# Kernel optimization log

Measured on AMD Instinct MI355X. Metric: run time of the kernel, lower is better.

The kernel has to match this reference:

```python
import jax, jax.numpy as jnp
import numpy as np

N_HEAD = 16


def setup_inputs() -> dict:
    key = jax.random.key(0)
    k1, k2, k3 = jax.random.split(key, 3)
    B, S, D = 2, 2048, 1024
    return {
        "hidden_states": jax.random.normal(k1, (B, S, D), dtype=jnp.float32),
        "c_attn_w": jax.random.normal(k2, (D, 3 * D), dtype=jnp.float32) * 0.02,
        "c_attn_b": jnp.zeros((3 * D,), dtype=jnp.float32),
        "c_proj_w": jax.random.normal(k3, (D, D), dtype=jnp.float32) * 0.02,
        "c_proj_b": jnp.zeros((D,), dtype=jnp.float32),
    }


def reference(hidden_states, c_attn_w, c_attn_b, c_proj_w, c_proj_b):
    B, S, D = hidden_states.shape
    H = N_HEAD
    hd = D // H
    # Fused QKV projection (Conv1D == linear with transposed weight layout)
    qkv = hidden_states @ c_attn_w + c_attn_b  # [B,S,3D]
    q, k, v = jnp.split(qkv, 3, axis=-1)
    # split heads -> [B,H,S,hd]
    q = q.reshape(B, S, H, hd).transpose(0, 2, 1, 3)
    k = k.reshape(B, S, H, hd).transpose(0, 2, 1, 3)
    v = v.reshape(B, S, H, hd).transpose(0, 2, 1, 3)
    # scaled dot-product with causal mask
    scores = jnp.einsum("bhqd,bhkd->bhqk", q, k) / jnp.asarray(hd ** 0.5, q.dtype)
    causal = jnp.tril(jnp.ones((S, S), dtype=bool))  # [S,S]
    mask_value = jnp.finfo(scores.dtype).min
    scores = jnp.where(causal[None, None, :, :], scores, mask_value)
    attn_weights = jax.nn.softmax(scores, axis=-1)  # [B,H,S,S]
    ctx = jnp.einsum("bhqk,bhkd->bhqd", attn_weights, v)  # [B,H,S,hd]
    ctx = ctx.transpose(0, 2, 1, 3).reshape(B, S, D)  # merge heads
    out = ctx @ c_proj_w + c_proj_b  # [B,S,D]
    return out
```

## Files before the change

### kernel.cpp

```cpp
#include <hip/hip_runtime.h>
#include <hip/hip_bf16.h>

typedef __attribute__((ext_vector_type(8))) short short8;
typedef __attribute__((ext_vector_type(4))) float f32x4;
typedef __attribute__((ext_vector_type(16))) float f32x16;
typedef __attribute__((ext_vector_type(4))) unsigned short u16x4;
typedef __attribute__((ext_vector_type(4))) unsigned int u32x4;

#define MFMA16(a, b, c) __builtin_amdgcn_mfma_f32_16x16x32_bf16((a), (b), (c), 0, 0, 0)
#define MFMA32(a, b, c) __builtin_amdgcn_mfma_f32_32x32x16_bf16((a), (b), (c), 0, 0, 0)

__device__ __forceinline__ unsigned short f2bf(float f) {
    union { float f; unsigned u; } v; v.f = f;
    return (unsigned short)((v.u + 0x7fffu + ((v.u >> 16) & 1u)) >> 16);
}

__device__ __forceinline__ unsigned cvtpk(float lo, float hi_) {
    unsigned r;
    asm volatile("v_cvt_pk_bf16_f32 %0, %1, %2" : "=v"(r) : "v"(lo), "v"(hi_));
    return r;
}

__global__ void cast_x_kernel(const float* __restrict__ x, ushort* __restrict__ y) {
    int i = blockIdx.x * blockDim.x + threadIdx.x;
    float4 v = ((const float4*)x)[i];
    u16x4 o = { f2bf(v.x), f2bf(v.y), f2bf(v.z), f2bf(v.w) };
    *(u16x4*)(y + (size_t)i * 4) = o;
}

__global__ void transpose_cast_kernel(const float* __restrict__ W, ushort* __restrict__ WT,
                                      int K, int N) {
    __shared__ ushort t[64][66];
    int n0 = blockIdx.x * 64, k0 = blockIdx.y * 64;
    int tn = threadIdx.x & 63, tg = threadIdx.x >> 6;
#pragma unroll
    for (int i = 0; i < 16; ++i) {
        int k = tg * 16 + i;
        t[tn][k] = f2bf(W[(size_t)(k0 + k) * N + n0 + tn]);
    }
    __syncthreads();
#pragma unroll
    for (int i = 0; i < 16; ++i) {
        int nn = tg * 16 + i;
        WT[(size_t)(n0 + nn) * K + k0 + tn] = t[nn][tn];
    }
}

#define QSCALE 0.18033688011112042f

template <int MODE>
__global__ __launch_bounds__(256, 3)
void gemm_bt_kernel(const ushort* __restrict__ A, const ushort* __restrict__ BT,
                    const float* __restrict__ bias,
                    ushort* __restrict__ Qb, ushort* __restrict__ Kb,
                    ushort* __restrict__ VT, float* __restrict__ Out,
                    int M, int N, int K) {
    __shared__ ushort Asm[2][128 * 32];
    __shared__ ushort Bsm[2][128 * 32];
    const int tid = threadIdx.x;
    const int lane = tid & 63;
    const int wv = tid >> 6;
    const int l15 = lane & 15, lg = lane >> 4;
    const int rm = (wv >> 1) * 64, cn = (wv & 1) * 64;
    const int row0 = blockIdx.y * 128, col0 = blockIdx.x * 128;

    const char* Agb = (const char*)(A + (size_t)row0 * K);
    const char* Bgb = (const char*)(BT + (size_t)col0 * K);
    const size_t rowbytes = (size_t)K * 2;

    f32x4 acc[4][4];
#pragma unroll
    for (int mi = 0; mi < 4; ++mi)
#pragma unroll
        for (int ni = 0; ni < 4; ++ni) acc[mi][ni] = f32x4{0.f, 0.f, 0.f, 0.f};

    const int sr0 = tid >> 2, sc0 = (tid & 3) ^ (sr0 & 3);
    const int sr1 = (tid + 256) >> 2, sc1 = (tid & 3) ^ (sr1 & 3);

#define GSTAGE(buf, k0_)                                                                \
    do {                                                                                \
        size_t kbyte = (size_t)(k0_)*2;                                                 \
        __builtin_amdgcn_global_load_lds(                                               \
            (const __attribute__((address_space(1))) void*)(Agb + (size_t)sr0 *         \
                rowbytes + kbyte + sc0 * 16),                                           \
            (__attribute__((address_space(3))) void*)((char*)&Asm[buf][0] + tid * 16),  \
            16, 0, 0);                                                                  \
        __builtin_amdgcn_global_load_lds(                                               \
            (const __attribute__((address_space(1))) void*)(Agb + (size_t)sr1 *         \
                rowbytes + kbyte + sc1 * 16),                                           \
            (__attribute__((address_space(3))) void*)((char*)&Asm[buf][0] + 4096 +      \
                tid * 16),                                                              \
            16, 0, 0);                                                                  \
        __builtin_amdgcn_global_load_lds(                                               \
            (const __attribute__((address_space(1))) void*)(Bgb + (size_t)sr0 *         \
                rowbytes + kbyte + sc0 * 16),                                           \
            (__attribute__((address_space(3))) void*)((char*)&Bsm[buf][0] + tid * 16),  \
            16, 0, 0);                                                                  \
        __builtin_amdgcn_global_load_lds(                                               \
            (const __attribute__((address_space(1))) void*)(Bgb + (size_t)sr1 *         \
                rowbytes + kbyte + sc1 * 16),                                           \
            (__attribute__((address_space(3))) void*)((char*)&Bsm[buf][0] + 4096 +      \
                tid * 16),                                                              \
            16, 0, 0);                                                                  \
    } while (0)

    GSTAGE(0, 0);
    __syncthreads();

    const int sw8 = (lg ^ (l15 & 3)) << 3;

    int cur = 0;
    for (int k0 = 0; k0 < K; k0 += 32) {
        if (k0 + 32 < K) GSTAGE(cur ^ 1, k0 + 32);
        short8 af[4], bf[4];
#pragma unroll
        for (int mi = 0; mi < 4; ++mi)
            af[mi] = *(const short8*)&Asm[cur][(rm + mi * 16 + l15) * 32 + sw8];
#pragma unroll
        for (int ni = 0; ni < 4; ++ni)
            bf[ni] = *(const short8*)&Bsm[cur][(cn + ni * 16 + l15) * 32 + sw8];
        __builtin_amdgcn_s_setprio(1);
#pragma unroll
        for (int mi = 0; mi < 4; ++mi)
#pragma unroll
            for (int ni = 0; ni < 4; ++ni)
                acc[mi][ni] = MFMA16(af[mi], bf[ni], acc[mi][ni]);
        __builtin_amdgcn_s_setprio(0);
        __syncthreads();
        cur ^= 1;
    }
#undef GSTAGE

    if (MODE == 0) {
        const int sect = col0 >> 10;
#pragma unroll
        for (int ni = 0; ni < 4; ++ni) {
            int col = col0 + cn + ni * 16 + l15;
            float bv = bias[col];
            int dcol = col & 1023, h = dcol >> 6, dd = dcol & 63;
#pragma unroll
            for (int mi = 0; mi < 4; ++mi) {
                int mrow0 = row0 + rm + mi * 16 + lg * 4;
                if (sect == 2) {
                    int b = mrow0 >> 11, s = mrow0 & 2047;
                    u16x4 o;
#pragma unroll
                    for (int j = 0; j < 4; ++j) o[j] = f2bf(acc[mi][ni][j] + bv);
                    *(u16x4*)&VT[((size_t)((b << 4) + h) * 64 + dd) * 2048 + s] = o;
                } else {
                    ushort* dst = sect ? Kb : Qb;
                    float sc = sect ? 1.f : QSCALE;
#pragma unroll
                    for (int j = 0; j < 4; ++j) {
                        int tok = mrow0 + j;
                        int b = tok >> 11, s = tok & 2047;
                        dst[((size_t)((b << 4) + h) * 2048 + s) * 64 + dd] =
                            f2bf((acc[mi][ni][j] + bv) * sc);
                    }
                }
            }
        }
    } else {
#pragma unroll
        for (int ni = 0; ni < 4; ++ni) {
            int col = col0 + cn + ni * 16 + l15;
            float bv = bias[col];
#pragma unroll
            for (int mi = 0; mi < 4; ++mi) {
                int mrow0 = row0 + rm + mi * 16 + lg * 4;
#pragma unroll
                for (int j = 0; j < 4; ++j)
                    Out[(size_t)(mrow0 + j) * N + col] = acc[mi][ni][j] + bv;
            }
        }
    }
}

template <int SPLIT>
__global__ __launch_bounds__(256, 4)
void attn_kernel(const ushort* __restrict__ Qb, const ushort* __restrict__ Kb,
                 const ushort* __restrict__ VT, ushort* __restrict__ CTX,
                 float* __restrict__ OP, float* __restrict__ ML) {
    __shared__ __align__(16) ushort Ksm[2][64 * 64];
    __shared__ __align__(16) ushort Vsm[2][64 * 64];

    const int tid = threadIdx.x;
    const int lane = tid & 63;
    const int w = tid >> 6;
    const int l31 = lane & 31;
    const int hi = lane >> 5;
    const int r7 = l31 & 7;

    const int id = blockIdx.x;
    int bh, qt, half, cBeg, cEnd;
    if (SPLIT) {
        const int xcd = id & 7, jj = id >> 3;
        bh = (xcd << 2) + (jj & 3);
        const int r = jj >> 2;
        half = r >> 4;
        const int s = r & 15;
        qt = (s < 8) ? s : 23 - s;
        cBeg = half * (qt + 1);
        cEnd = cBeg + (qt + 1);
    } else {
        const int xcd = id & 7, jj = id >> 3;
        bh = (xcd << 2) + (jj >> 4);
        qt = ((jj >> 5) & 1) ? (jj & 15) : 15 - (jj & 15);
        half = 0; cBeg = 0; cEnd = 2 * qt + 2;
    }
    const int nc = 2 * qt + 2;
    const int qw0 = qt * 128 + w * 32;
    const int qrow = qw0 + l31;

    const ushort* Qh = Qb + (size_t)bh * 2048 * 64;
    const ushort* Kh = Kb + (size_t)bh * 2048 * 64;
    const ushort* Vh = VT + (size_t)bh * 64 * 2048;

    short8 qf[4];
#pragma unroll
    for (int dc = 0; dc < 4; ++dc)
        qf[dc] = *(const short8*)&Qh[(size_t)qrow * 64 + dc * 16 + hi * 8];

    const int srow = tid >> 3;
    const int sxor = ((tid & 7) ^ (srow & 7)) * 8;

#define GLL(src, dst) __builtin_amdgcn_global_load_lds(                                 \
        (const __attribute__((address_space(1))) void*)(src),                           \
        (__attribute__((address_space(3))) void*)(dst), 16, 0, 0)

#define STAGE(buf, kb_)                                                                 \
    do {                                                                                \
        const ushort* kp = Kh + (size_t)((kb_) + srow) * 64 + sxor;                     \
        GLL(kp, (char*)&Ksm[buf][0] + tid * 16);                                        \
        GLL(kp + 32 * 64, (char*)&Ksm[buf][0] + 4096 + tid * 16);                       \
        const ushort* vp = Vh + (size_t)srow * 2048 + (kb_) + sxor;                     \
        GLL(vp, (char*)&Vsm[buf][0] + tid * 16);                                        \
        GLL(vp + (size_t)32 * 2048, (char*)&Vsm[buf][0] + 4096 + tid * 16);             \
    } while (0)

    const int cdiag = 2 * qt + (w >> 1);

    STAGE(0, cBeg * 64);
    __syncthreads();

    float mrun = -1e30f, lsum = 0.f;
    f32x16 acc0, acc1;
#pragma unroll
    for (int r = 0; r < 16; ++r) { acc0[r] = 0.f; acc1[r] = 0.f; }

    int cur = 0;
    for (int c = cBeg; c < cEnd; ++c) {
        const int kb = c * 64;
        if (c + 1 < cEnd) STAGE(cur ^ 1, kb + 64);

        if (!(w < 2 && c == nc - 1)) {
            const ushort* Kc = &Ksm[cur][0];
            const ushort* Vc = &Vsm[cur][0];

            f32x16 st0, st1;
#pragma unroll
            for (int r = 0; r < 16; ++r) { st0[r] = 0.f; st1[r] = 0.f; }
            __builtin_amdgcn_s_setprio(1);
#pragma unroll
            for (int dc = 0; dc < 4; ++dc) {
                short8 kf0 = *(const short8*)(Kc + l31 * 64 + (((dc * 2 + hi) ^ r7) << 3));
                short8 kf1 = *(const short8*)(Kc + (32 + l31) * 64 + (((dc * 2 + hi) ^ r7) << 3));
                st0 = MFMA32(kf0, qf[dc], st0);
                st1 = MFMA32(kf1, qf[dc], st1);
            }
            __builtin_amdgcn_s_setprio(0);

            if (c == cdiag) {
                const int base0 = kb + (hi << 2);
                const int base1 = kb + 32 + (hi << 2);
#pragma unroll
                for (int r = 0; r < 16; ++r) {
                    int k0 = base0 + ((r & 3) + 8 * (r >> 2));
                    int k1 = base1 + ((r & 3) + 8 * (r >> 2));
                    st0[r] = (k0 <= qrow) ? st0[r] : -1e30f;
                    st1[r] = (k1 <= qrow) ? st1[r] : -1e30f;
                }
            }

            float tm[8];
#pragma unroll
            for (int i = 0; i < 8; ++i)
                tm[i] = fmaxf(fmaxf(st0[i], st0[i + 8]), fmaxf(st1[i], st1[i + 8]));
            float tmax = fmaxf(fmaxf(fmaxf(tm[0], tm[1]), fmaxf(tm[2], tm[3])),
                               fmaxf(fmaxf(tm[4], tm[5]), fmaxf(tm[6], tm[7])));
            tmax = fmaxf(tmax, __shfl_xor(tmax, 32));

            if (!__all(tmax <= mrun + 8.0f)) {
                float mnew = fmaxf(mrun, tmax);
                float sc = exp2f(mrun - mnew);
#pragma unroll
                for (int r = 0; r < 16; ++r) { acc0[r] *= sc; acc1[r] *= sc; }
                lsum *= sc;
                mrun = mnew;
            }

#pragma unroll
            for (int r = 0; r < 16; ++r) st0[r] = exp2f(st0[r] - mrun);
#pragma unroll
            for (int r = 0; r < 16; ++r) st1[r] = exp2f(st1[r] - mrun);
            float ts[8];
#pragma unroll
            for (int i = 0; i < 8; ++i) ts[i] = st0[i] + st0[i + 8];
#pragma unroll
            for (int i = 0; i < 8; ++i) ts[i] += st1[i] + st1[i + 8];
            float tsum = ((ts[0] + ts[1]) + (ts[2] + ts[3])) +
                         ((ts[4] + ts[5]) + (ts[6] + ts[7]));
            lsum += tsum;

#define MAKE_PFRAG(st, kcL, out)                                                        \
    do {                                                                                \
        unsigned a0 = cvtpk(st[8 * kcL + 0], st[8 * kcL + 1]);                          \
        unsigned a1 = cvtpk(st[8 * kcL + 2], st[8 * kcL + 3]);                          \
        unsigned b0 = cvtpk(st[8 * kcL + 4], st[8 * kcL + 5]);                          \
        unsigned b1 = cvtpk(st[8 * kcL + 6], st[8 * kcL + 7]);                          \
        asm volatile("v_permlane32_swap_b32 %0, %1" : "+v"(a0), "+v"(b0));              \
        asm volatile("v_permlane32_swap_b32 %0, %1" : "+v"(a1), "+v"(b1));              \
        u32x4 fw;                                                                       \
        fw.x = a0; fw.y = a1; fw.z = b0; fw.w = b1;                                     \
        out = __builtin_bit_cast(short8, fw);                                           \
    } while (0)

#define PV_GROUP(st, kcL, g)                                                            \
    do {                                                                                \
        short8 pf;                                                                      \
        MAKE_PFRAG(st, kcL, pf);                                                        \
        short8 v0 = *(const short8*)(Vc + l31 * 64 + (((2 * (g) + hi) ^ r7) << 3));     \
        short8 v1 = *(const short8*)(Vc + (32 + l31) * 64 +                             \
                                     (((2 * (g) + hi) ^ r7) << 3));                     \
        acc0 = MFMA32(v0, pf, acc0);                                                    \
        acc1 = MFMA32(v1, pf, acc1);                                                    \
    } while (0)

            __builtin_amdgcn_s_setprio(1);
            PV_GROUP(st0, 0, 0);
            PV_GROUP(st0, 1, 1);
            PV_GROUP(st1, 0, 2);
            PV_GROUP(st1, 1, 3);
            __builtin_amdgcn_s_setprio(0);
#undef PV_GROUP
#undef MAKE_PFRAG
        }

        __syncthreads();
        cur ^= 1;
    }
#undef STAGE
#undef GLL

    lsum += __shfl_xor(lsum, 32);

    if (SPLIT) {
        const int pidx = ((bh << 4) + qt) * 2 + half;
        float* op = OP + (size_t)pidx * 8192 + (size_t)(w * 32 + l31) * 64;
#define WRITE_PART(accv, dt)                                                            \
    do {                                                                                \
        _Pragma("unroll")                                                               \
        for (int q2 = 0; q2 < 4; ++q2) {                                                \
            int d0 = dt * 32 + 8 * q2 + (hi << 2);                                      \
            f32x4 o = { accv[4 * q2 + 0], accv[4 * q2 + 1],                             \
                        accv[4 * q2 + 2], accv[4 * q2 + 3] };                           \
            *(f32x4*)&op[d0] = o;                                                       \
        }                                                                               \
    } while (0)
        WRITE_PART(acc0, 0);
        WRITE_PART(acc1, 1);
#undef WRITE_PART
        if (hi == 0) {
            float2 r2 = { mrun, lsum };
            *(float2*)&ML[((size_t)pidx * 128 + w * 32 + l31) * 2] = r2;
        }
    } else {
        const float inv = 1.f / lsum;
        const int b = bh >> 4, h = bh & 15;
        const size_t tokrow = ((size_t)b * 2048 + qw0 + l31) * 1024 + (size_t)h * 64;
#define WRITE_DT(accv, dt)                                                              \
    do {                                                                                \
        _Pragma("unroll")                                                               \
        for (int q2 = 0; q2 < 4; ++q2) {                                                \
            int d0 = dt * 32 + 8 * q2 + (hi << 2);                                      \
            u16x4 o;                                                                    \
            _Pragma("unroll")                                                           \
            for (int j = 0; j < 4; ++j) o[j] = f2bf(accv[4 * q2 + j] * inv);            \
            *(u16x4*)&CTX[tokrow + d0] = o;                                             \
        }                                                                               \
    } while (0)
        WRITE_DT(acc0, 0);
        WRITE_DT(acc1, 1);
#undef WRITE_DT
    }
}

__global__ __launch_bounds__(256)
void merge_kernel(const float* __restrict__ OP, const float* __restrict__ ML,
                  ushort* __restrict__ CTX) {
    const int bid = blockIdx.x;
    const int bh = bid >> 4, qt = bid & 15;
    const int tid = threadIdx.x;
    const int row = tid >> 1, dh = (tid & 1) << 5;
    const size_t p0 = (size_t)bid * 2, p1 = p0 + 1;
    const float2 ml0 = *(const float2*)&ML[(p0 * 128 + row) * 2];
    const float2 ml1 = *(const float2*)&ML[(p1 * 128 + row) * 2];
    const float M = fmaxf(ml0.x, ml1.x);
    const float f0 = exp2f(ml0.x - M), f1 = exp2f(ml1.x - M);
    const float inv = 1.f / (f0 * ml0.y + f1 * ml1.y);
    const float* a0 = OP + p0 * 8192 + (size_t)row * 64 + dh;
    const float* a1 = OP + p1 * 8192 + (size_t)row * 64 + dh;
    const size_t tok = (size_t)(bh >> 4) * 2048 + qt * 128 + row;
    ushort* dst = CTX + tok * 1024 + (size_t)(bh & 15) * 64 + dh;
#pragma unroll
    for (int k = 0; k < 8; ++k) {
        f32x4 v0 = *(const f32x4*)(a0 + 4 * k);
        f32x4 v1 = *(const f32x4*)(a1 + 4 * k);
        u16x4 o;
#pragma unroll
        for (int j = 0; j < 4; ++j) o[j] = f2bf((f0 * v0[j] + f1 * v1[j]) * inv);
        *(u16x4*)(dst + 4 * k) = o;
    }
}

extern "C" void kernel_launch(void* const* d_in, const int* in_sizes, int n_in,
                              void* d_out, int out_size, void* d_ws, size_t ws_size,
                              hipStream_t stream) {
    const float* X     = (const float*)d_in[0];
    const float* Wqkv  = (const float*)d_in[1];
    const float* bqkv  = (const float*)d_in[2];
    const float* Wproj = (const float*)d_in[3];
    const float* bproj = (const float*)d_in[4];
    float* Out = (float*)d_out;

    ushort* Xb     = (ushort*)d_ws;
    ushort* WqkvT  = Xb + (size_t)4096 * 1024;
    ushort* WprojT = WqkvT + (size_t)3072 * 1024;
    ushort* Qb     = WprojT + (size_t)1024 * 1024;
    ushort* Kb     = Qb + (size_t)4096 * 1024;
    ushort* VT     = Kb + (size_t)4096 * 1024;
    ushort* CTX    = VT + (size_t)4096 * 1024;
    float* OP = (float*)((char*)d_ws + (size_t)48 * 1024 * 1024);
    float* ML = OP + (size_t)1024 * 128 * 64;
    const size_t NEED = (size_t)(48 + 32 + 1) * 1024 * 1024;

    cast_x_kernel<<<4096, 256, 0, stream>>>(X, Xb);
    transpose_cast_kernel<<<dim3(48, 16), 256, 0, stream>>>(Wqkv, WqkvT, 1024, 3072);
    transpose_cast_kernel<<<dim3(16, 16), 256, 0, stream>>>(Wproj, WprojT, 1024, 1024);
    gemm_bt_kernel<0><<<dim3(24, 32), 256, 0, stream>>>(Xb, WqkvT, bqkv, Qb, Kb, VT, nullptr,
                                                        4096, 3072, 1024);
    if (ws_size >= NEED) {
        attn_kernel<1><<<1024, 256, 0, stream>>>(Qb, Kb, VT, CTX, OP, ML);
        merge_kernel<<<512, 256, 0, stream>>>(OP, ML, CTX);
    } else {
        attn_kernel<0><<<512, 256, 0, stream>>>(Qb, Kb, VT, CTX, nullptr, nullptr);
    }
    gemm_bt_kernel<1><<<dim3(8, 32), 256, 0, stream>>>(CTX, WprojT, bproj, nullptr, nullptr,
                                                       nullptr, Out, 4096, 1024, 1024);
}
```

Measured before the change: 131.6 us.

## Triple-buffer GEMM loads, store split-attention partials in bf16, vectorize merge

The GEMM main loop moves from double to triple-buffered LDS staging. It uses explicit vmcnt waits and a single barrier per iteration, so global loads run two stages ahead of the MFMA work. The split-K attention partial outputs are now written as bf16 instead of fp32, which halves the traffic to and from the partial buffer. The merge kernel is rewritten to use 16-byte vector loads and stores. In exchange, partials lose precision before the merge, and the GEMM uses more LDS, which may reduce occupancy.

```diff
diff --git a/kernel.cpp b/kernel.cpp
--- a/kernel.cpp
+++ b/kernel.cpp
@@ -5,6 +5,7 @@
 typedef __attribute__((ext_vector_type(4))) float f32x4;
 typedef __attribute__((ext_vector_type(16))) float f32x16;
 typedef __attribute__((ext_vector_type(4))) unsigned short u16x4;
+typedef __attribute__((ext_vector_type(8))) unsigned short u16x8;
 typedef __attribute__((ext_vector_type(4))) unsigned int u32x4;
 
 #define MFMA16(a, b, c) __builtin_amdgcn_mfma_f32_16x16x32_bf16((a), (b), (c), 0, 0, 0)
@@ -13,6 +14,11 @@
 __device__ __forceinline__ unsigned short f2bf(float f) {
     union { float f; unsigned u; } v; v.f = f;
     return (unsigned short)((v.u + 0x7fffu + ((v.u >> 16) & 1u)) >> 16);
+}
+
+__device__ __forceinline__ float bf2f(unsigned short s) {
+    union { unsigned u; float f; } v; v.u = (unsigned)s << 16;
+    return v.f;
 }
 
 __device__ __forceinline__ unsigned cvtpk(float lo, float hi_) {
@@ -55,8 +61,8 @@
                     ushort* __restrict__ Qb, ushort* __restrict__ Kb,
                     ushort* __restrict__ VT, float* __restrict__ Out,
                     int M, int N, int K) {
-    __shared__ ushort Asm[2][128 * 32];
-    __shared__ ushort Bsm[2][128 * 32];
+    __shared__ ushort Asm[3][128 * 32];
+    __shared__ ushort Bsm[3][128 * 32];
     const int tid = threadIdx.x;
     const int lane = tid & 63;
     const int wv = tid >> 6;
@@ -104,14 +110,18 @@
             16, 0, 0);                                                                  \
     } while (0)
 
+    const int NK = K >> 5;
     GSTAGE(0, 0);
-    __syncthreads();
+    GSTAGE(1, 32);
 
     const int sw8 = (lg ^ (l15 & 3)) << 3;
 
-    int cur = 0;
-    for (int k0 = 0; k0 < K; k0 += 32) {
-        if (k0 + 32 < K) GSTAGE(cur ^ 1, k0 + 32);
+    int cur = 0, stg = 2;
+    for (int i = 0; i < NK; ++i) {
+        if (i < NK - 1) asm volatile("s_waitcnt vmcnt(4)" ::: "memory");
+        else            asm volatile("s_waitcnt vmcnt(0)" ::: "memory");
+        __builtin_amdgcn_s_barrier();
+        if (i + 2 < NK) GSTAGE(stg, (i + 2) * 32);
         short8 af[4], bf[4];
 #pragma unroll
         for (int mi = 0; mi < 4; ++mi)
@@ -126,8 +136,8 @@
             for (int ni = 0; ni < 4; ++ni)
                 acc[mi][ni] = MFMA16(af[mi], bf[ni], acc[mi][ni]);
         __builtin_amdgcn_s_setprio(0);
-        __syncthreads();
-        cur ^= 1;
+        cur = (cur == 2) ? 0 : cur + 1;
+        stg = (stg == 2) ? 0 : stg + 1;
     }
 #undef GSTAGE
 
@@ -180,7 +190,7 @@
 __global__ __launch_bounds__(256, 4)
 void attn_kernel(const ushort* __restrict__ Qb, const ushort* __restrict__ Kb,
                  const ushort* __restrict__ VT, ushort* __restrict__ CTX,
-                 float* __restrict__ OP, float* __restrict__ ML) {
+                 ushort* __restrict__ OP, float* __restrict__ ML) {
     __shared__ __align__(16) ushort Ksm[2][64 * 64];
     __shared__ __align__(16) ushort Vsm[2][64 * 64];
 
@@ -356,15 +366,16 @@
 
     if (SPLIT) {
         const int pidx = ((bh << 4) + qt) * 2 + half;
-        float* op = OP + (size_t)pidx * 8192 + (size_t)(w * 32 + l31) * 64;
+        ushort* op = OP + (size_t)pidx * 8192 + (size_t)(w * 32 + l31) * 64;
 #define WRITE_PART(accv, dt)                                                            \
     do {                                                                                \
         _Pragma("unroll")                                                               \
         for (int q2 = 0; q2 < 4; ++q2) {                                                \
             int d0 = dt * 32 + 8 * q2 + (hi << 2);                                      \
-            f32x4 o = { accv[4 * q2 + 0], accv[4 * q2 + 1],                             \
-                        accv[4 * q2 + 2], accv[4 * q2 + 3] };                           \
-            *(f32x4*)&op[d0] = o;                                                       \
+            u16x4 o;                                                                    \
+            _Pragma("unroll")                                                           \
+            for (int j = 0; j < 4; ++j) o[j] = f2bf(accv[4 * q2 + j]);                  \
+            *(u16x4*)&op[d0] = o;                                                       \
         }                                                                               \
     } while (0)
         WRITE_PART(acc0, 0);
@@ -396,30 +407,30 @@
 }
 
 __global__ __launch_bounds__(256)
-void merge_kernel(const float* __restrict__ OP, const float* __restrict__ ML,
+void merge_kernel(const ushort* __restrict__ OP, const float* __restrict__ ML,
                   ushort* __restrict__ CTX) {
     const int bid = blockIdx.x;
     const int bh = bid >> 4, qt = bid & 15;
     const int tid = threadIdx.x;
-    const int row = tid >> 1, dh = (tid & 1) << 5;
-    const size_t p0 = (size_t)bid * 2, p1 = p0 + 1;
-    const float2 ml0 = *(const float2*)&ML[(p0 * 128 + row) * 2];
-    const float2 ml1 = *(const float2*)&ML[(p1 * 128 + row) * 2];
-    const float M = fmaxf(ml0.x, ml1.x);
-    const float f0 = exp2f(ml0.x - M), f1 = exp2f(ml1.x - M);
-    const float inv = 1.f / (f0 * ml0.y + f1 * ml1.y);
-    const float* a0 = OP + p0 * 8192 + (size_t)row * 64 + dh;
-    const float* a1 = OP + p1 * 8192 + (size_t)row * 64 + dh;
-    const size_t tok = (size_t)(bh >> 4) * 2048 + qt * 128 + row;
-    ushort* dst = CTX + tok * 1024 + (size_t)(bh & 15) * 64 + dh;
-#pragma unroll
-    for (int k = 0; k < 8; ++k) {
-        f32x4 v0 = *(const f32x4*)(a0 + 4 * k);
-        f32x4 v1 = *(const f32x4*)(a1 + 4 * k);
-        u16x4 o;
-#pragma unroll
-        for (int j = 0; j < 4; ++j) o[j] = f2bf((f0 * v0[j] + f1 * v1[j]) * inv);
-        *(u16x4*)(dst + 4 * k) = o;
+    const size_t base0 = (size_t)(bid * 2) * 8192;
+    const size_t mlb = (size_t)(bid * 2) * 128;
+#pragma unroll
+    for (int it = 0; it < 4; ++it) {
+        const int g = tid + it * 256;
+        const int row = g >> 3, d0 = (g & 7) * 8;
+        const float2 ml0 = *(const float2*)&ML[(mlb + row) * 2];
+        const float2 ml1 = *(const float2*)&ML[(mlb + 128 + row) * 2];
+        const float M = fmaxf(ml0.x, ml1.x);
+        const float f0 = exp2f(ml0.x - M), f1 = exp2f(ml1.x - M);
+        const float inv = 1.f / (f0 * ml0.y + f1 * ml1.y);
+        const u16x8 a0 = *(const u16x8*)&OP[base0 + (size_t)g * 8];
+        const u16x8 a1 = *(const u16x8*)&OP[base0 + 8192 + (size_t)g * 8];
+        u16x8 o;
+#pragma unroll
+        for (int j = 0; j < 8; ++j)
+            o[j] = f2bf((f0 * bf2f(a0[j]) + f1 * bf2f(a1[j])) * inv);
+        const size_t tok = (size_t)(bh >> 4) * 2048 + qt * 128 + row;
+        *(u16x8*)&CTX[tok * 1024 + (size_t)(bh & 15) * 64 + d0] = o;
     }
 }
 
@@ -440,9 +451,9 @@
     ushort* Kb     = Qb + (size_t)4096 * 1024;
     ushort* VT     = Kb + (size_t)4096 * 1024;
     ushort* CTX    = VT + (size_t)4096 * 1024;
-    float* OP = (float*)((char*)d_ws + (size_t)48 * 1024 * 1024);
-    float* ML = OP + (size_t)1024 * 128 * 64;
-    const size_t NEED = (size_t)(48 + 32 + 1) * 1024 * 1024;
+    ushort* OP = (ushort*)((char*)d_ws + (size_t)48 * 1024 * 1024);
+    float*  ML = (float*)(OP + (size_t)1024 * 128 * 64);
+    const size_t NEED = (size_t)(48 + 16 + 1) * 1024 * 1024;
 
     cast_x_kernel<<<4096, 256, 0, stream>>>(X, Xb);
     transpose_cast_kernel<<<dim3(48, 16), 256, 0, stream>>>(Wqkv, WqkvT, 1024, 3072);
```

New measurement: 124.7 us. -5.2%, faster.
